# Kernel tuning notes

Hardware: AMD Instinct MI355X
Metric: run time of the kernel (lower is better)

The kernel has to match this reference:

```python
import jax, jax.numpy as jnp
import numpy as np

B, S, H = 4, 2048, 1024

def setup_inputs() -> dict:
    key = jax.random.key(0)
    k = jax.random.split(key, 5)
    scale = 1.0 / np.sqrt(H)
    return {
        "hidden": jax.random.normal(k[0], (B, S, H), dtype=jnp.float32),
        "mask": jnp.zeros((B, 1, S, S), dtype=jnp.float32),
        "R": jax.random.normal(k[1], (S, S), dtype=jnp.float32),
        "G_w": jax.random.normal(k[2], (H, H), dtype=jnp.float32) * scale,
        "G_b": jnp.zeros((H,), dtype=jnp.float32),
        "F_w": jax.random.normal(k[3], (H, H), dtype=jnp.float32) * scale,
        "F_b": jnp.zeros((H,), dtype=jnp.float32),
    }

def reference(hidden, mask, R, G_w, G_b, F_w, F_b):
    # scores: [B, S, S] = learned random bias + additive attention mask
    scores = R + mask[:, 0]
    probs = jax.nn.softmax(scores, axis=-1)  # dropout is identity in eval mode
    values = jnp.einsum('bsh,oh->bso', hidden, G_w) + G_b  # G_linear
    out = jnp.einsum('bqk,bkh->bqh', probs, values)
    out = jnp.einsum('bsh,oh->bso', out, F_w) + F_b  # final_linear
    return out
```

## Files before the change

kernel.cpp:

```cpp
#include <hip/hip_runtime.h>
#include <hip/hip_bf16.h>

typedef __bf16 bf16x8 __attribute__((ext_vector_type(8)));
typedef __bf16 bf16x4 __attribute__((ext_vector_type(4)));
typedef float  f32x4  __attribute__((ext_vector_type(4)));
typedef float  f32x16 __attribute__((ext_vector_type(16)));

#define GPTR(p) ((__attribute__((address_space(1))) void*)(p))
#define LPTR(p) ((__attribute__((address_space(3))) void*)(p))

__global__ __launch_bounds__(256) void phase_a_kernel(
    const float* __restrict__ hidden, __bf16* __restrict__ h_bf,
    const float* __restrict__ Fw, __bf16* __restrict__ f_bf,
    const float* __restrict__ Gw, __bf16* __restrict__ gt_bf,
    const float* __restrict__ Gb, const float* __restrict__ Fb,
    float* __restrict__ b2, int H) {
    __shared__ float tile[64][65];
    const int blk = blockIdx.x;
    const int t = threadIdx.x;

    if (blk < 4096) {
        long i = ((long)blk * 256 + t) * 8;
        float4 a = *reinterpret_cast<const float4*>(hidden + i);
        float4 c = *reinterpret_cast<const float4*>(hidden + i + 4);
        bf16x8 o;
        o[0] = (__bf16)a.x; o[1] = (__bf16)a.y; o[2] = (__bf16)a.z; o[3] = (__bf16)a.w;
        o[4] = (__bf16)c.x; o[5] = (__bf16)c.y; o[6] = (__bf16)c.z; o[7] = (__bf16)c.w;
        *reinterpret_cast<bf16x8*>(h_bf + i) = o;
    } else if (blk < 4608) {
        long i = ((long)(blk - 4096) * 256 + t) * 8;
        float4 a = *reinterpret_cast<const float4*>(Fw + i);
        float4 c = *reinterpret_cast<const float4*>(Fw + i + 4);
        bf16x8 o;
        o[0] = (__bf16)a.x; o[1] = (__bf16)a.y; o[2] = (__bf16)a.z; o[3] = (__bf16)a.w;
        o[4] = (__bf16)c.x; o[5] = (__bf16)c.y; o[6] = (__bf16)c.z; o[7] = (__bf16)c.w;
        *reinterpret_cast<bf16x8*>(f_bf + i) = o;
    } else if (blk < 4864) {
        const int id = blk - 4608;
        const int bx = (id & 15) * 64;
        const int by = (id >> 4) * 64;
        const int tr = t >> 4;
        const int tc = (t & 15) * 4;
#pragma unroll
        for (int i = 0; i < 4; i++) {
            float4 v = *reinterpret_cast<const float4*>(&Gw[(size_t)(by + tr + i * 16) * H + bx + tc]);
            tile[tr + i * 16][tc + 0] = v.x;
            tile[tr + i * 16][tc + 1] = v.y;
            tile[tr + i * 16][tc + 2] = v.z;
            tile[tr + i * 16][tc + 3] = v.w;
        }
        __syncthreads();
        const int wr = t >> 2;
        const int wc = (t & 3) * 16;
        bf16x8 o0, o1;
#pragma unroll
        for (int j = 0; j < 8; j++) o0[j] = (__bf16)tile[wc + j][wr];
#pragma unroll
        for (int j = 0; j < 8; j++) o1[j] = (__bf16)tile[wc + 8 + j][wr];
        *reinterpret_cast<bf16x8*>(&gt_bf[(size_t)(bx + wr) * H + by + wc]) = o0;
        *reinterpret_cast<bf16x8*>(&gt_bf[(size_t)(bx + wr) * H + by + wc + 8]) = o1;
    } else {
        const int o = blk - 4864;
        float s = 0.f;
        for (int h = t; h < H; h += 256) s += Fw[(size_t)o * H + h] * Gb[h];
#pragma unroll
        for (int off = 32; off > 0; off >>= 1) s += __shfl_xor(s, off);
        __shared__ float ss[4];
        if ((t & 63) == 0) ss[t >> 6] = s;
        __syncthreads();
        if (t == 0) b2[o] = ss[0] + ss[1] + ss[2] + ss[3] + Fb[o];
    }
}

__global__ __launch_bounds__(256) void phase_b_kernel(
    const __bf16* __restrict__ f_bf, const __bf16* __restrict__ gt_bf,
    __bf16* __restrict__ Wm, const float* __restrict__ R,
    const float* __restrict__ mask, __bf16* __restrict__ P, int H, int S) {
    const int blk = blockIdx.x;
    const int t = threadIdx.x;

    if (blk < 256) {
        __shared__ __bf16 As[64 * 64];
        __shared__ __bf16 Bs[64 * 64];
        const int lane = t & 63;
        const int wave = t >> 6;
        const int lane31 = lane & 31;
        const int hi = lane >> 5;
        const int wm = (wave >> 1) * 32;
        const int wn = (wave & 1) * 32;
        const int bm = (blk >> 4) * 64;
        const int bn = (blk & 15) * 64;

        const int rsub = lane >> 3;
        const int csub = lane & 7;
        const int lchunk = csub ^ rsub;
        const __bf16* ga0 = f_bf + (size_t)(bm + wave * 16 + rsub) * H + lchunk * 8;
        const __bf16* gb0 = gt_bf + (size_t)(bn + wave * 16 + rsub) * H + lchunk * 8;

        f32x16 acc = (f32x16)(0.f);
        for (int kt = 0; kt < H; kt += 64) {
            __syncthreads();
#pragma unroll
            for (int c = 0; c < 2; c++)
                __builtin_amdgcn_global_load_lds(GPTR(ga0 + (size_t)(c * 8) * H + kt),
                                                 LPTR(&As[(wave * 16 + c * 8) * 64]), 16, 0, 0);
#pragma unroll
            for (int c = 0; c < 2; c++)
                __builtin_amdgcn_global_load_lds(GPTR(gb0 + (size_t)(c * 8) * H + kt),
                                                 LPTR(&Bs[(wave * 16 + c * 8) * 64]), 16, 0, 0);
            __syncthreads();
#pragma unroll
            for (int s = 0; s < 4; s++) {
                const int ra = wm + lane31;
                const int rb = wn + lane31;
                bf16x8 af = *reinterpret_cast<const bf16x8*>(
                    &As[ra * 64 + (((2 * s + hi) ^ (ra & 7)) << 3)]);
                bf16x8 bfr = *reinterpret_cast<const bf16x8*>(
                    &Bs[rb * 64 + (((2 * s + hi) ^ (rb & 7)) << 3)]);
                acc = __builtin_amdgcn_mfma_f32_32x32x16_bf16(af, bfr, acc, 0, 0, 0);
            }
        }
        const int cm = bm + wm;
        const int cn = bn + wn + lane31;
#pragma unroll
        for (int rq = 0; rq < 4; rq++) {
            const int rbase = rq * 8 + 4 * hi;
#pragma unroll
            for (int rr = 0; rr < 4; rr++)
                Wm[(size_t)(cm + rbase + rr) * H + cn] = (__bf16)acc[rq * 4 + rr];
        }
    } else {
        const int id = blk - 256;
        const int b = id >> 11;
        const int q = id & 2047;
        const int lane = t & 63, wave = t >> 6;
        const float* rrow = R + (size_t)q * S;
        const float* mrow = mask + ((size_t)b * S + q) * (size_t)S;
        __bf16* prow = P + ((size_t)b * S + q) * (size_t)S;

        float v[8];
#pragma unroll
        for (int i = 0; i < 2; i++) {
            float4 r4 = *reinterpret_cast<const float4*>(rrow + t * 8 + i * 4);
            float4 m4 = *reinterpret_cast<const float4*>(mrow + t * 8 + i * 4);
            v[i * 4 + 0] = r4.x + m4.x;
            v[i * 4 + 1] = r4.y + m4.y;
            v[i * 4 + 2] = r4.z + m4.z;
            v[i * 4 + 3] = r4.w + m4.w;
        }
        float mx = v[0];
#pragma unroll
        for (int i = 1; i < 8; i++) mx = fmaxf(mx, v[i]);
#pragma unroll
        for (int off = 32; off > 0; off >>= 1) mx = fmaxf(mx, __shfl_xor(mx, off));
        __shared__ float smax[4], ssum[4];
        if (lane == 0) smax[wave] = mx;
        __syncthreads();
        mx = fmaxf(fmaxf(smax[0], smax[1]), fmaxf(smax[2], smax[3]));
        float sum = 0.f;
#pragma unroll
        for (int i = 0; i < 8; i++) { v[i] = __expf(v[i] - mx); sum += v[i]; }
#pragma unroll
        for (int off = 32; off > 0; off >>= 1) sum += __shfl_xor(sum, off);
        if (lane == 0) ssum[wave] = sum;
        __syncthreads();
        sum = ssum[0] + ssum[1] + ssum[2] + ssum[3];
        const float inv = 1.0f / sum;
        bf16x8 o;
#pragma unroll
        for (int i = 0; i < 8; i++) o[i] = (__bf16)(v[i] * inv);
        *reinterpret_cast<bf16x8*>(prow + t * 8) = o;
    }
}

template <bool TRANSC, bool CFLOAT, bool BIAS, bool SWZ>
__global__ __launch_bounds__(256) void gemm_nt_kernel(
    const __bf16* __restrict__ A, const __bf16* __restrict__ B,
    const float* __restrict__ bias, void* __restrict__ Cv,
    int K, int lda, int ldb, int ldc,
    long strideA, long strideB, long strideC) {
    const int t = threadIdx.x;
    const int lane = t & 63;
    const int wave = t >> 6;
    const int lane31 = lane & 31;
    const int hi = lane >> 5;
    const int wm = (wave >> 1) * 64;
    const int wn = (wave & 1) * 64;
    int bm, bn, bz;
    if constexpr (SWZ) {
        const int id = blockIdx.x;
        const int xcd = id & 7;
        const int slot = id >> 3;
        bz = xcd >> 1;
        bm = ((xcd & 1) * 8 + (slot >> 3)) * 128;
        bn = (slot & 7) * 128;
    } else {
        bm = blockIdx.y * 128;
        bn = blockIdx.x * 128;
        bz = blockIdx.z;
    }

    A += (size_t)bz * strideA;
    B += (size_t)bz * strideB;

    __shared__ __bf16 smem[TRANSC ? 16640 : 16384];
    __bf16* As = smem;
    __bf16* Bs = smem + 8192;

    const int rsub = lane >> 3;
    const int csub = lane & 7;
    const int lchunk = csub ^ rsub;
    const __bf16* ga0 = A + (size_t)(bm + wave * 32 + rsub) * lda + lchunk * 8;
    const __bf16* gb0 = B + (size_t)(bn + wave * 32 + rsub) * ldb + lchunk * 8;

    f32x16 acc[2][2];
#pragma unroll
    for (int i = 0; i < 2; i++)
#pragma unroll
        for (int j = 0; j < 2; j++) acc[i][j] = (f32x16)(0.f);

    for (int kt = 0; kt < K; kt += 64) {
        __syncthreads();
#pragma unroll
        for (int c = 0; c < 4; c++)
            __builtin_amdgcn_global_load_lds(GPTR(ga0 + (size_t)(c * 8) * lda + kt),
                                             LPTR(&As[(wave * 32 + c * 8) * 64]), 16, 0, 0);
#pragma unroll
        for (int c = 0; c < 4; c++)
            __builtin_amdgcn_global_load_lds(GPTR(gb0 + (size_t)(c * 8) * ldb + kt),
                                             LPTR(&Bs[(wave * 32 + c * 8) * 64]), 16, 0, 0);
        __syncthreads();
#pragma unroll
        for (int s = 0; s < 4; s++) {
            bf16x8 af[2], bfr[2];
#pragma unroll
            for (int mi = 0; mi < 2; mi++) {
                const int r = wm + mi * 32 + lane31;
                af[mi] = *reinterpret_cast<const bf16x8*>(
                    &As[r * 64 + (((2 * s + hi) ^ (r & 7)) << 3)]);
            }
#pragma unroll
            for (int ni = 0; ni < 2; ni++) {
                const int r = wn + ni * 32 + lane31;
                bfr[ni] = *reinterpret_cast<const bf16x8*>(
                    &Bs[r * 64 + (((2 * s + hi) ^ (r & 7)) << 3)]);
            }
#pragma unroll
            for (int mi = 0; mi < 2; mi++)
#pragma unroll
                for (int ni = 0; ni < 2; ni++)
                    acc[mi][ni] = __builtin_amdgcn_mfma_f32_32x32x16_bf16(af[mi], bfr[ni], acc[mi][ni], 0, 0, 0);
        }
    }

    if constexpr (TRANSC) {
        __syncthreads();
        __bf16* sC = smem;
#pragma unroll
        for (int mi = 0; mi < 2; mi++)
#pragma unroll
            for (int ni = 0; ni < 2; ni++)
#pragma unroll
                for (int rq = 0; rq < 4; rq++) {
                    const int n_l = wn + ni * 32 + lane31;
                    const int m_l = wm + mi * 32 + rq * 8 + 4 * hi;
                    bf16x4 pk;
#pragma unroll
                    for (int rr = 0; rr < 4; rr++) pk[rr] = (__bf16)acc[mi][ni][rq * 4 + rr];
                    *reinterpret_cast<bf16x4*>(&sC[n_l * 130 + m_l]) = pk;
                }
        __syncthreads();
        __bf16* Ct = (__bf16*)Cv + (size_t)bz * strideC;
        const int col = (t & 15) * 8;
#pragma unroll
        for (int p = 0; p < 8; p++) {
            const int row = p * 16 + (t >> 4);
            bf16x8 v = *reinterpret_cast<const bf16x8*>(&sC[row * 130 + col]);
            *reinterpret_cast<bf16x8*>(Ct + (size_t)(bn + row) * ldc + bm + col) = v;
        }
    } else {
        __bf16* Cb = (__bf16*)Cv + (size_t)bz * strideC;
        float* Cf = (float*)Cv + (size_t)bz * strideC;
#pragma unroll
        for (int mi = 0; mi < 2; mi++)
#pragma unroll
            for (int ni = 0; ni < 2; ni++) {
                const int cm = bm + wm + mi * 32;
                const int cn = bn + wn + ni * 32 + lane31;
                const float bv = BIAS ? bias[cn] : 0.0f;
#pragma unroll
                for (int rq = 0; rq < 4; rq++) {
                    const int rbase = rq * 8 + 4 * hi;
                    if constexpr (CFLOAT) {
#pragma unroll
                        for (int rr = 0; rr < 4; rr++)
                            Cf[(size_t)(cm + rbase + rr) * ldc + cn] = acc[mi][ni][rq * 4 + rr] + bv;
                    } else {
#pragma unroll
                        for (int rr = 0; rr < 4; rr++)
                            Cb[(size_t)(cm + rbase + rr) * ldc + cn] = (__bf16)(acc[mi][ni][rq * 4 + rr] + bv);
                    }
                }
            }
    }
}

extern "C" void kernel_launch(void* const* d_in, const int* in_sizes, int n_in,
                              void* d_out, int out_size, void* d_ws, size_t ws_size,
                              hipStream_t stream) {
    const float* hidden = (const float*)d_in[0];
    const float* mask   = (const float*)d_in[1];
    const float* R      = (const float*)d_in[2];
    const float* G_w    = (const float*)d_in[3];
    const float* G_b    = (const float*)d_in[4];
    const float* F_w    = (const float*)d_in[5];
    const float* F_b    = (const float*)d_in[6];
    float* out = (float*)d_out;

    constexpr int B = 4, S = 2048, H = 1024;
    char* ws = (char*)d_ws;
    __bf16* h_bf  = (__bf16*)(ws);
    __bf16* vt    = (__bf16*)(ws + (16ll << 20));
    __bf16* probs = (__bf16*)(ws + (32ll << 20));
    __bf16* f_bf  = (__bf16*)(ws + (64ll << 20));
    __bf16* gt_bf = (__bf16*)(ws + (66ll << 20));
    __bf16* Wm    = (__bf16*)(ws + (68ll << 20));
    float*  b2    = (float*)(ws + (70ll << 20));

    phase_a_kernel<<<5888, 256, 0, stream>>>(hidden, h_bf, F_w, f_bf, G_w, gt_bf,
                                             G_b, F_b, b2, H);

    phase_b_kernel<<<256 + B * S, 256, 0, stream>>>(f_bf, gt_bf, Wm, R, mask, probs, H, S);

    gemm_nt_kernel<true, false, false, false><<<dim3(H / 128, S / 128, B), 256, 0, stream>>>(
        h_bf, Wm, nullptr, vt, H, H, H,  S,
        (long)S * H, 0, (long)H * S);

    gemm_nt_kernel<false, true, true, true><<<512, 256, 0, stream>>>(
        probs, vt, b2, out, S, S, S, H,
        (long)S * S, (long)H * S, (long)S * H);
}
```

Measured before the change: 241.1 us.

## Double-buffer GEMM LDS tiles and store fragments in MFMA-ready layout

The GEMM main loop gains two LDS buffers, so the next K-tile is fetched with global_load_lds while MFMAs run on the current one, and one of the two barriers per iteration goes away. The LDS layout also changes from XOR-swizzled rows to a fragment-major layout, where each lane's 16-byte chunk lands exactly where the matching MFMA operand read expects it. This keeps the reads contiguous and conflict-free. In exchange LDS use doubles to 64 KB per block, which may lower occupancy, and the global reads now come from 32 rows per wave instruction rather than 8, which may hurt coalescing.

Measured after the change: 280.6 us. 16.4% more time.

```diff
diff --git a/kernel.cpp b/kernel.cpp
--- a/kernel.cpp
+++ b/kernel.cpp
@@ -3,7 +3,6 @@
 
 typedef __bf16 bf16x8 __attribute__((ext_vector_type(8)));
 typedef __bf16 bf16x4 __attribute__((ext_vector_type(4)));
-typedef float  f32x4  __attribute__((ext_vector_type(4)));
 typedef float  f32x16 __attribute__((ext_vector_type(16)));
 
 #define GPTR(p) ((__attribute__((address_space(1))) void*)(p))
@@ -203,15 +202,22 @@
     A += (size_t)bz * strideA;
     B += (size_t)bz * strideB;
 
-    __shared__ __bf16 smem[TRANSC ? 16640 : 16384];
-    __bf16* As = smem;
-    __bf16* Bs = smem + 8192;
-
-    const int rsub = lane >> 3;
-    const int csub = lane & 7;
-    const int lchunk = csub ^ rsub;
-    const __bf16* ga0 = A + (size_t)(bm + wave * 32 + rsub) * lda + lchunk * 8;
-    const __bf16* gb0 = B + (size_t)(bn + wave * 32 + rsub) * ldb + lchunk * 8;
+    __shared__ __bf16 smem[32768];
+    __bf16* const Abuf = smem;
+    __bf16* const Bbuf = smem + 16384;
+
+    const __bf16* gA = A + (size_t)(bm + wave * 32 + lane31) * lda + hi * 8;
+    const __bf16* gB = B + (size_t)(bn + wave * 32 + lane31) * ldb + hi * 8;
+
+    auto stage = [&](int p, int kt) {
+#pragma unroll
+        for (int s = 0; s < 4; s++) {
+            __builtin_amdgcn_global_load_lds(GPTR(gA + kt + s * 16),
+                                             LPTR(Abuf + p * 8192 + (s * 4 + wave) * 512), 16, 0, 0);
+            __builtin_amdgcn_global_load_lds(GPTR(gB + kt + s * 16),
+                                             LPTR(Bbuf + p * 8192 + (s * 4 + wave) * 512), 16, 0, 0);
+        }
+    };
 
     f32x16 acc[2][2];
 #pragma unroll
@@ -219,42 +225,35 @@
 #pragma unroll
         for (int j = 0; j < 2; j++) acc[i][j] = (f32x16)(0.f);
 
+    stage(0, 0);
+    __syncthreads();
+    int p = 0;
     for (int kt = 0; kt < K; kt += 64) {
-        __syncthreads();
-#pragma unroll
-        for (int c = 0; c < 4; c++)
-            __builtin_amdgcn_global_load_lds(GPTR(ga0 + (size_t)(c * 8) * lda + kt),
-                                             LPTR(&As[(wave * 32 + c * 8) * 64]), 16, 0, 0);
-#pragma unroll
-        for (int c = 0; c < 4; c++)
-            __builtin_amdgcn_global_load_lds(GPTR(gb0 + (size_t)(c * 8) * ldb + kt),
-                                             LPTR(&Bs[(wave * 32 + c * 8) * 64]), 16, 0, 0);
-        __syncthreads();
+        if (kt + 64 < K) stage(p ^ 1, kt + 64);
+        const __bf16* Ap = Abuf + p * 8192;
+        const __bf16* Bp = Bbuf + p * 8192;
 #pragma unroll
         for (int s = 0; s < 4; s++) {
             bf16x8 af[2], bfr[2];
 #pragma unroll
-            for (int mi = 0; mi < 2; mi++) {
-                const int r = wm + mi * 32 + lane31;
+            for (int mi = 0; mi < 2; mi++)
                 af[mi] = *reinterpret_cast<const bf16x8*>(
-                    &As[r * 64 + (((2 * s + hi) ^ (r & 7)) << 3)]);
-            }
-#pragma unroll
-            for (int ni = 0; ni < 2; ni++) {
-                const int r = wn + ni * 32 + lane31;
+                    &Ap[((s * 4 + (wave >> 1) * 2 + mi) * 64 + lane) * 8]);
+#pragma unroll
+            for (int ni = 0; ni < 2; ni++)
                 bfr[ni] = *reinterpret_cast<const bf16x8*>(
-                    &Bs[r * 64 + (((2 * s + hi) ^ (r & 7)) << 3)]);
-            }
+                    &Bp[((s * 4 + (wave & 1) * 2 + ni) * 64 + lane) * 8]);
 #pragma unroll
             for (int mi = 0; mi < 2; mi++)
 #pragma unroll
                 for (int ni = 0; ni < 2; ni++)
                     acc[mi][ni] = __builtin_amdgcn_mfma_f32_32x32x16_bf16(af[mi], bfr[ni], acc[mi][ni], 0, 0, 0);
         }
+        __syncthreads();
+        p ^= 1;
     }
 
     if constexpr (TRANSC) {
-        __syncthreads();
         __bf16* sC = smem;
 #pragma unroll
         for (int mi = 0; mi < 2; mi++)
@@ -273,8 +272,8 @@
         __bf16* Ct = (__bf16*)Cv + (size_t)bz * strideC;
         const int col = (t & 15) * 8;
 #pragma unroll
-        for (int p = 0; p < 8; p++) {
-            const int row = p * 16 + (t >> 4);
+        for (int pp = 0; pp < 8; pp++) {
+            const int row = pp * 16 + (t >> 4);
             bf16x8 v = *reinterpret_cast<const bf16x8*>(&sC[row * 130 + col]);
             *reinterpret_cast<bf16x8*>(Ct + (size_t)(bn + row) * ldc + bm + col) = v;
         }
```
